# Kernel tuning notes

Measured on AMD Instinct MI355X. Metric: run time of the kernel, lower is better.

## Reference

```python
import jax, jax.numpy as jnp
import numpy as np

N_NODES = 100000
N_EDGES = 50000
NNZ = 1600000
D = 128
L = 2


def setup_inputs() -> dict:
    key = jax.random.key(0)
    ks = jax.random.split(key, 8)
    x = jax.random.normal(ks[0], (N_NODES, D), dtype=jnp.float32)
    e = jax.random.normal(ks[1], (N_EDGES, D), dtype=jnp.float32)
    node_idx = jax.random.randint(ks[2], (NNZ,), 0, N_NODES)
    edge_idx = jax.random.randint(ks[3], (NNZ,), 0, N_EDGES)
    hyperedge_index = jnp.stack([node_idx, edge_idx]).astype(jnp.int64)
    # per-layer params: node linear, edge linear, bias; shared PReLU slope a (init 0.25)
    Wn = jax.random.normal(ks[4], (L, D, D), dtype=jnp.float32) / np.sqrt(D)
    We = jax.random.normal(ks[5], (L, D, D), dtype=jnp.float32) / np.sqrt(D)
    b = jnp.zeros((L, D), dtype=jnp.float32)
    a = jnp.array(0.25, dtype=jnp.float32)
    return {"x": x, "e": e, "hyperedge_index": hyperedge_index,
            "num_nodes": N_NODES, "num_edges": N_EDGES,
            "Wn": Wn, "We": We, "b": b, "a": a}


def reference(x, e, hyperedge_index, num_nodes, num_edges, Wn, We, b, a):
    node_idx = hyperedge_index[0]
    edge_idx = hyperedge_index[1]
    ones = jnp.ones(node_idx.shape, x.dtype)
    deg_e = jax.ops.segment_sum(ones, edge_idx, num_segments=num_edges)  # B (edge degree)
    deg_v = jax.ops.segment_sum(ones, node_idx, num_segments=num_nodes)  # D_v (node degree)
    inv_e = jnp.where(deg_e > 0, 1.0 / deg_e, 0.0)[:, None]
    inv_v = jnp.where(deg_v > 0, 1.0 / deg_v, 0.0)[:, None]
    num_layers = Wn.shape[0]
    for l in range(num_layers):
        x1 = x @ Wn[l]                                   # [N, D]
        # gather node feats per incidence, mean-aggregate onto hyperedges
        m = jax.ops.segment_sum(x1[node_idx], edge_idx, num_segments=num_edges) * inv_e  # [E, D]
        h = m + e @ We[l] + b[l]                          # hyperedge hidden [E, D]
        # scatter hyperedge messages back to nodes, degree-normalized
        x = jax.ops.segment_sum(h[edge_idx], node_idx, num_segments=num_nodes) * inv_v   # [N, D]
        x = jnp.where(x >= 0, x, a * x)                   # shared PReLU
    return x
```

## Files before the change

### kernel.cpp

```cpp
#include <hip/hip_runtime.h>

#define DD 128


__global__ __launch_bounds__(256) void hist_kernel(const int* __restrict__ nidx,
                                                   const int* __restrict__ eidx,
                                                   int* __restrict__ cnt_v,
                                                   int* __restrict__ cnt_e, int nnz) {
  int i = blockIdx.x * 256 + threadIdx.x;
  if (i < nnz) {
    atomicAdd(&cnt_v[nidx[i]], 1);
    atomicAdd(&cnt_e[eidx[i]], 1);
  }
}

__global__ __launch_bounds__(256) void partial_reduce(const int* __restrict__ cnt, int n,
                                                      int* __restrict__ partials) {
  __shared__ int s[256];
  int t = threadIdx.x;
  int base = blockIdx.x * 1024;
  int sum = 0;
#pragma unroll
  for (int k = 0; k < 4; ++k) {
    int i = base + t * 4 + k;
    if (i < n) sum += cnt[i];
  }
  s[t] = sum;
  __syncthreads();
  for (int o = 128; o > 0; o >>= 1) {
    if (t < o) s[t] += s[t + o];
    __syncthreads();
  }
  if (t == 0) partials[blockIdx.x] = s[0];
}

__global__ __launch_bounds__(256) void scan_partials(int* __restrict__ partials, int nparts,
                                                     int* __restrict__ rp, int n) {
  __shared__ int s[256];
  int t = threadIdx.x;
  int v = (t < nparts) ? partials[t] : 0;
  s[t] = v;
  __syncthreads();
  for (int o = 1; o < 256; o <<= 1) {
    int add = (t >= o) ? s[t - o] : 0;
    __syncthreads();
    s[t] += add;
    __syncthreads();
  }
  if (t < nparts) partials[t] = s[t] - v;
  if (t == 255) rp[n] = s[255];
}

__global__ __launch_bounds__(256) void scan_final(const int* __restrict__ cnt,
                                                  const int* __restrict__ partials, int n,
                                                  int* __restrict__ rp, int* __restrict__ cur) {
  __shared__ int s[256];
  int t = threadIdx.x;
  int base = blockIdx.x * 1024;
  int v[4];
  int sum = 0;
#pragma unroll
  for (int k = 0; k < 4; ++k) {
    int i = base + t * 4 + k;
    v[k] = (i < n) ? cnt[i] : 0;
    sum += v[k];
  }
  s[t] = sum;
  __syncthreads();
  int own = sum;
  for (int o = 1; o < 256; o <<= 1) {
    int add = (t >= o) ? s[t - o] : 0;
    __syncthreads();
    s[t] += add;
    __syncthreads();
  }
  int off = partials[blockIdx.x] + (s[t] - own);
#pragma unroll
  for (int k = 0; k < 4; ++k) {
    int i = base + t * 4 + k;
    if (i < n) {
      rp[i] = off;
      cur[i] = off;
      off += v[k];
    }
  }
}

__global__ __launch_bounds__(256) void fill_kernel(const int* __restrict__ nidx,
                                                   const int* __restrict__ eidx,
                                                   int* __restrict__ cur_v,
                                                   int* __restrict__ cur_e,
                                                   int* __restrict__ col_v,
                                                   int* __restrict__ col_e, int nnz) {
  int i = blockIdx.x * 256 + threadIdx.x;
  if (i < nnz) {
    int v = nidx[i], e = eidx[i];
    int p = atomicAdd(&cur_e[e], 1);
    col_e[p] = v;
    int q = atomicAdd(&cur_v[v], 1);
    col_v[q] = e;
  }
}


__global__ __launch_bounds__(256) void gather_mean(const float* __restrict__ src,
                                                   const int* __restrict__ rp,
                                                   const int* __restrict__ col,
                                                   float* __restrict__ dst, int nrows) {
  int r = blockIdx.x * 4 + (threadIdx.x >> 6);
  if (r >= nrows) return;
  int lane = threadIdx.x & 63;
  int beg = rp[r], end = rp[r + 1];
  float ax = 0.f, ay = 0.f;
  int j = beg;
  for (; j + 4 <= end; j += 4) {
    int s0 = col[j], s1 = col[j + 1], s2 = col[j + 2], s3 = col[j + 3];
    float2 v0 = ((const float2*)(src + (size_t)s0 * DD))[lane];
    float2 v1 = ((const float2*)(src + (size_t)s1 * DD))[lane];
    float2 v2 = ((const float2*)(src + (size_t)s2 * DD))[lane];
    float2 v3 = ((const float2*)(src + (size_t)s3 * DD))[lane];
    ax += v0.x + v1.x + v2.x + v3.x;
    ay += v0.y + v1.y + v2.y + v3.y;
  }
  for (; j < end; ++j) {
    int s = col[j];
    float2 v = ((const float2*)(src + (size_t)s * DD))[lane];
    ax += v.x;
    ay += v.y;
  }
  float inv = (end > beg) ? 1.f / (float)(end - beg) : 0.f;
  float2 o;
  o.x = ax * inv;
  o.y = ay * inv;
  ((float2*)(dst + (size_t)r * DD))[lane] = o;
}

__global__ __launch_bounds__(256) void gather_prelu(const float* __restrict__ src,
                                                    const int* __restrict__ rp,
                                                    const int* __restrict__ col,
                                                    const float* __restrict__ a_ptr,
                                                    float* __restrict__ dst, int nrows) {
  int r = blockIdx.x * 4 + (threadIdx.x >> 6);
  if (r >= nrows) return;
  int lane = threadIdx.x & 63;
  int beg = rp[r], end = rp[r + 1];
  float ax = 0.f, ay = 0.f;
  int j = beg;
  for (; j + 4 <= end; j += 4) {
    int s0 = col[j], s1 = col[j + 1], s2 = col[j + 2], s3 = col[j + 3];
    float2 v0 = ((const float2*)(src + (size_t)s0 * DD))[lane];
    float2 v1 = ((const float2*)(src + (size_t)s1 * DD))[lane];
    float2 v2 = ((const float2*)(src + (size_t)s2 * DD))[lane];
    float2 v3 = ((const float2*)(src + (size_t)s3 * DD))[lane];
    ax += v0.x + v1.x + v2.x + v3.x;
    ay += v0.y + v1.y + v2.y + v3.y;
  }
  for (; j < end; ++j) {
    int s = col[j];
    float2 v = ((const float2*)(src + (size_t)s * DD))[lane];
    ax += v.x;
    ay += v.y;
  }
  float inv = (end > beg) ? 1.f / (float)(end - beg) : 0.f;
  float a = a_ptr[0];
  ax *= inv;
  ay *= inv;
  ax = ax >= 0.f ? ax : a * ax;
  ay = ay >= 0.f ? ay : a * ay;
  float2 o;
  o.x = ax;
  o.y = ay;
  ((float2*)(dst + (size_t)r * DD))[lane] = o;
}

__global__ __launch_bounds__(128) void edge_mlp(const float* __restrict__ agg,
                                                const float* __restrict__ ein,
                                                const float* __restrict__ Wn,
                                                const float* __restrict__ We,
                                                const float* __restrict__ bias,
                                                float* __restrict__ h, int E) {
  const int ROWS = 8;
  __shared__ float sA[ROWS][DD];
  __shared__ float sE[ROWS][DD];
  int r0 = blockIdx.x * ROWS;
  int t = threadIdx.x;
#pragma unroll
  for (int r = 0; r < ROWS; ++r) {
    int row = r0 + r;
    if (row < E) {
      sA[r][t] = agg[(size_t)row * DD + t];
      sE[r][t] = ein[(size_t)row * DD + t];
    } else {
      sA[r][t] = 0.f;
      sE[r][t] = 0.f;
    }
  }
  __syncthreads();

  float acc[ROWS];
  float bv = bias[t];
#pragma unroll
  for (int r = 0; r < ROWS; ++r) acc[r] = bv;

  for (int k = 0; k < DD; ++k) {
    float wn = Wn[k * DD + t];
    float we = We[k * DD + t];
#pragma unroll
    for (int r = 0; r < ROWS; ++r) {
      acc[r] += sA[r][k] * wn + sE[r][k] * we;
    }
  }
#pragma unroll
  for (int r = 0; r < ROWS; ++r) {
    int row = r0 + r;
    if (row < E) h[(size_t)row * DD + t] = acc[r];
  }
}


extern "C" void kernel_launch(void* const* d_in, const int* in_sizes, int n_in,
                              void* d_out, int out_size, void* d_ws, size_t ws_size,
                              hipStream_t stream) {
  const float* x_in  = (const float*)d_in[0];
  const float* e_in  = (const float*)d_in[1];
  const int*   hidx  = (const int*)d_in[2];
  const float* Wn    = (const float*)d_in[5];
  const float* We    = (const float*)d_in[6];
  const float* bias  = (const float*)d_in[7];
  const float* a_ptr = (const float*)d_in[8];

  const int N   = in_sizes[0] / DD;
  const int E   = in_sizes[1] / DD;
  const int NNZ = in_sizes[2] / 2;
  const int L   = in_sizes[5] / (DD * DD);

  const int* node_idx = hidx;
  const int* edge_idx = hidx + NNZ;

  char* ws = (char*)d_ws;
  size_t off = 0;
  auto take = [&](size_t bytes) {
    void* p = ws + off;
    off = (off + bytes + 511) & ~(size_t)511;
    return p;
  };
  int* cnt_v  = (int*)take((size_t)N * 4);
  int* cnt_e  = (int*)take((size_t)E * 4);
  int* rp_v   = (int*)take((size_t)(N + 1) * 4);
  int* rp_e   = (int*)take((size_t)(E + 1) * 4);
  int* cur_v  = (int*)take((size_t)N * 4);
  int* cur_e  = (int*)take((size_t)E * 4);
  int* part_v = (int*)take(256 * 4);
  int* part_e = (int*)take(256 * 4);
  int* col_v  = (int*)take((size_t)NNZ * 4);
  int* col_e  = (int*)take((size_t)NNZ * 4);
  float* agg  = (float*)take((size_t)E * DD * 4);

  float* xbuf = (float*)d_out;

  const int nparts_v = (N + 1023) / 1024;
  const int nparts_e = (E + 1023) / 1024;

  hipMemsetAsync(cnt_v, 0, (size_t)N * 4, stream);
  hipMemsetAsync(cnt_e, 0, (size_t)E * 4, stream);
  hist_kernel<<<(NNZ + 255) / 256, 256, 0, stream>>>(node_idx, edge_idx, cnt_v, cnt_e, NNZ);

  partial_reduce<<<nparts_v, 256, 0, stream>>>(cnt_v, N, part_v);
  partial_reduce<<<nparts_e, 256, 0, stream>>>(cnt_e, E, part_e);
  scan_partials<<<1, 256, 0, stream>>>(part_v, nparts_v, rp_v, N);
  scan_partials<<<1, 256, 0, stream>>>(part_e, nparts_e, rp_e, E);
  scan_final<<<nparts_v, 256, 0, stream>>>(cnt_v, part_v, N, rp_v, cur_v);
  scan_final<<<nparts_e, 256, 0, stream>>>(cnt_e, part_e, E, rp_e, cur_e);

  fill_kernel<<<(NNZ + 255) / 256, 256, 0, stream>>>(node_idx, edge_idx, cur_v, cur_e,
                                                     col_v, col_e, NNZ);

  const float* x_src = x_in;
  for (int l = 0; l < L; ++l) {
    gather_mean<<<(E + 3) / 4, 256, 0, stream>>>(x_src, rp_e, col_e, agg, E);
    edge_mlp<<<(E + 7) / 8, 128, 0, stream>>>(agg, e_in,
                                              Wn + (size_t)l * DD * DD,
                                              We + (size_t)l * DD * DD,
                                              bias + (size_t)l * DD, agg, E);
    gather_prelu<<<(N + 3) / 4, 256, 0, stream>>>(agg, rp_v, col_v, a_ptr, xbuf, N);
    x_src = xbuf;
  }
}
```

Before: 1.189 ms.

## Fuse edge gather-mean into edge MLP and vectorize CSR build kernels

Merges the per-edge mean aggregation with the edge linear layer into one kernel, so each block gathers 16 aggregated rows straight into shared memory and computes the 2x4 register-tiled matmul, dropping the agg round trip through global memory. The histogram and CSR fill kernels now read four indices per thread with int4 loads. Both gather loops unroll to eight independent loads in flight. The per-block work grows and fewer blocks launch for the edge stage, which may reduce latency hiding in the gather.

New measurement: 1.170 ms. Within noise of the previous version (-1.7%).

```diff
diff --git a/kernel.cpp b/kernel.cpp
--- a/kernel.cpp
+++ b/kernel.cpp
@@ -7,10 +7,23 @@
                                                    const int* __restrict__ eidx,
                                                    int* __restrict__ cnt_v,
                                                    int* __restrict__ cnt_e, int nnz) {
-  int i = blockIdx.x * 256 + threadIdx.x;
-  if (i < nnz) {
-    atomicAdd(&cnt_v[nidx[i]], 1);
-    atomicAdd(&cnt_e[eidx[i]], 1);
+  int base = (blockIdx.x * 256 + threadIdx.x) * 4;
+  if (base + 4 <= nnz) {
+    int4 n4 = *reinterpret_cast<const int4*>(nidx + base);
+    int4 e4 = *reinterpret_cast<const int4*>(eidx + base);
+    atomicAdd(&cnt_v[n4.x], 1);
+    atomicAdd(&cnt_v[n4.y], 1);
+    atomicAdd(&cnt_v[n4.z], 1);
+    atomicAdd(&cnt_v[n4.w], 1);
+    atomicAdd(&cnt_e[e4.x], 1);
+    atomicAdd(&cnt_e[e4.y], 1);
+    atomicAdd(&cnt_e[e4.z], 1);
+    atomicAdd(&cnt_e[e4.w], 1);
+  } else {
+    for (int i = base; i < nnz; ++i) {
+      atomicAdd(&cnt_v[nidx[i]], 1);
+      atomicAdd(&cnt_e[eidx[i]], 1);
+    }
   }
 }
 
@@ -92,47 +105,113 @@
                                                    int* __restrict__ cur_e,
                                                    int* __restrict__ col_v,
                                                    int* __restrict__ col_e, int nnz) {
-  int i = blockIdx.x * 256 + threadIdx.x;
-  if (i < nnz) {
-    int v = nidx[i], e = eidx[i];
-    int p = atomicAdd(&cur_e[e], 1);
-    col_e[p] = v;
-    int q = atomicAdd(&cur_v[v], 1);
-    col_v[q] = e;
-  }
-}
-
-
-__global__ __launch_bounds__(256) void gather_mean(const float* __restrict__ src,
-                                                   const int* __restrict__ rp,
-                                                   const int* __restrict__ col,
-                                                   float* __restrict__ dst, int nrows) {
-  int r = blockIdx.x * 4 + (threadIdx.x >> 6);
-  if (r >= nrows) return;
+  int base = (blockIdx.x * 256 + threadIdx.x) * 4;
+  if (base + 4 <= nnz) {
+    int4 n4 = *reinterpret_cast<const int4*>(nidx + base);
+    int4 e4 = *reinterpret_cast<const int4*>(eidx + base);
+    int p;
+    p = atomicAdd(&cur_e[e4.x], 1); col_e[p] = n4.x;
+    p = atomicAdd(&cur_e[e4.y], 1); col_e[p] = n4.y;
+    p = atomicAdd(&cur_e[e4.z], 1); col_e[p] = n4.z;
+    p = atomicAdd(&cur_e[e4.w], 1); col_e[p] = n4.w;
+    p = atomicAdd(&cur_v[n4.x], 1); col_v[p] = e4.x;
+    p = atomicAdd(&cur_v[n4.y], 1); col_v[p] = e4.y;
+    p = atomicAdd(&cur_v[n4.z], 1); col_v[p] = e4.z;
+    p = atomicAdd(&cur_v[n4.w], 1); col_v[p] = e4.w;
+  } else {
+    for (int i = base; i < nnz; ++i) {
+      int v = nidx[i], e = eidx[i];
+      int p = atomicAdd(&cur_e[e], 1);
+      col_e[p] = v;
+      int q = atomicAdd(&cur_v[v], 1);
+      col_v[q] = e;
+    }
+  }
+}
+
+__global__ __launch_bounds__(256) void gather_mlp(const float* __restrict__ x,
+                                                  const int* __restrict__ rp,
+                                                  const int* __restrict__ col,
+                                                  const float* __restrict__ ein,
+                                                  const float* __restrict__ Wn,
+                                                  const float* __restrict__ We,
+                                                  const float* __restrict__ bias,
+                                                  float* __restrict__ h, int E) {
+  const int ROWS = 16;
+  __shared__ float sA[ROWS][DD];
+  __shared__ float sE[ROWS][DD];
+  int r0 = blockIdx.x * ROWS;
+  int wave = threadIdx.x >> 6;
   int lane = threadIdx.x & 63;
-  int beg = rp[r], end = rp[r + 1];
-  float ax = 0.f, ay = 0.f;
-  int j = beg;
-  for (; j + 4 <= end; j += 4) {
-    int s0 = col[j], s1 = col[j + 1], s2 = col[j + 2], s3 = col[j + 3];
-    float2 v0 = ((const float2*)(src + (size_t)s0 * DD))[lane];
-    float2 v1 = ((const float2*)(src + (size_t)s1 * DD))[lane];
-    float2 v2 = ((const float2*)(src + (size_t)s2 * DD))[lane];
-    float2 v3 = ((const float2*)(src + (size_t)s3 * DD))[lane];
-    ax += v0.x + v1.x + v2.x + v3.x;
-    ay += v0.y + v1.y + v2.y + v3.y;
-  }
-  for (; j < end; ++j) {
-    int s = col[j];
-    float2 v = ((const float2*)(src + (size_t)s * DD))[lane];
-    ax += v.x;
-    ay += v.y;
-  }
-  float inv = (end > beg) ? 1.f / (float)(end - beg) : 0.f;
-  float2 o;
-  o.x = ax * inv;
-  o.y = ay * inv;
-  ((float2*)(dst + (size_t)r * DD))[lane] = o;
+
+#pragma unroll
+  for (int rr = 0; rr < 4; ++rr) {
+    int li = wave * 4 + rr;
+    int row = r0 + li;
+    float ax = 0.f, ay = 0.f;
+    float2 ev = make_float2(0.f, 0.f);
+    if (row < E) {
+      int beg = rp[row], end = rp[row + 1];
+      int j = beg;
+      for (; j + 8 <= end; j += 8) {
+        int c[8];
+#pragma unroll
+        for (int u = 0; u < 8; ++u) c[u] = col[j + u];
+#pragma unroll
+        for (int u = 0; u < 8; ++u) {
+          float2 v = ((const float2*)(x + (size_t)c[u] * DD))[lane];
+          ax += v.x;
+          ay += v.y;
+        }
+      }
+      for (; j < end; ++j) {
+        float2 v = ((const float2*)(x + (size_t)col[j] * DD))[lane];
+        ax += v.x;
+        ay += v.y;
+      }
+      float inv = (end > beg) ? 1.f / (float)(end - beg) : 0.f;
+      ax *= inv;
+      ay *= inv;
+      ev = ((const float2*)(ein + (size_t)row * DD))[lane];
+    }
+    ((float2*)&sA[li][0])[lane] = make_float2(ax, ay);
+    ((float2*)&sE[li][0])[lane] = ev;
+  }
+  __syncthreads();
+
+  int rg = threadIdx.x >> 5;
+  int rA = rg * 2, rB = rA + 1;
+  int c0 = (threadIdx.x & 31) * 4;
+  float acc0[4], acc1[4];
+#pragma unroll
+  for (int cc = 0; cc < 4; ++cc) {
+    float bv = bias[c0 + cc];
+    acc0[cc] = bv;
+    acc1[cc] = bv;
+  }
+  for (int k0 = 0; k0 < DD; k0 += 4) {
+    float aA[4], aB[4], eA[4], eB[4];
+    *(float4*)aA = *(const float4*)&sA[rA][k0];
+    *(float4*)aB = *(const float4*)&sA[rB][k0];
+    *(float4*)eA = *(const float4*)&sE[rA][k0];
+    *(float4*)eB = *(const float4*)&sE[rB][k0];
+#pragma unroll
+    for (int kk = 0; kk < 4; ++kk) {
+      float wn[4], we[4];
+      *(float4*)wn = *(const float4*)&Wn[(size_t)(k0 + kk) * DD + c0];
+      *(float4*)we = *(const float4*)&We[(size_t)(k0 + kk) * DD + c0];
+#pragma unroll
+      for (int cc = 0; cc < 4; ++cc) {
+        acc0[cc] += aA[kk] * wn[cc] + eA[kk] * we[cc];
+        acc1[cc] += aB[kk] * wn[cc] + eB[kk] * we[cc];
+      }
+    }
+  }
+  int rowA = r0 + rA, rowB = r0 + rB;
+  if (rowA < E)
+    *(float4*)&h[(size_t)rowA * DD + c0] = make_float4(acc0[0], acc0[1], acc0[2], acc0[3]);
+  if (rowB < E)
+    *(float4*)&h[(size_t)rowB * DD + c0] = make_float4(acc1[0], acc1[1], acc1[2], acc1[3]);
 }
 
 __global__ __launch_bounds__(256) void gather_prelu(const float* __restrict__ src,
@@ -146,18 +225,19 @@
   int beg = rp[r], end = rp[r + 1];
   float ax = 0.f, ay = 0.f;
   int j = beg;
-  for (; j + 4 <= end; j += 4) {
-    int s0 = col[j], s1 = col[j + 1], s2 = col[j + 2], s3 = col[j + 3];
-    float2 v0 = ((const float2*)(src + (size_t)s0 * DD))[lane];
-    float2 v1 = ((const float2*)(src + (size_t)s1 * DD))[lane];
-    float2 v2 = ((const float2*)(src + (size_t)s2 * DD))[lane];
-    float2 v3 = ((const float2*)(src + (size_t)s3 * DD))[lane];
-    ax += v0.x + v1.x + v2.x + v3.x;
-    ay += v0.y + v1.y + v2.y + v3.y;
+  for (; j + 8 <= end; j += 8) {
+    int c[8];
+#pragma unroll
+    for (int u = 0; u < 8; ++u) c[u] = col[j + u];
+#pragma unroll
+    for (int u = 0; u < 8; ++u) {
+      float2 v = ((const float2*)(src + (size_t)c[u] * DD))[lane];
+      ax += v.x;
+      ay += v.y;
+    }
   }
   for (; j < end; ++j) {
-    int s = col[j];
-    float2 v = ((const float2*)(src + (size_t)s * DD))[lane];
+    float2 v = ((const float2*)(src + (size_t)col[j] * DD))[lane];
     ax += v.x;
     ay += v.y;
   }
@@ -167,54 +247,7 @@
   ay *= inv;
   ax = ax >= 0.f ? ax : a * ax;
   ay = ay >= 0.f ? ay : a * ay;
-  float2 o;
-  o.x = ax;
-  o.y = ay;
-  ((float2*)(dst + (size_t)r * DD))[lane] = o;
-}
-
-__global__ __launch_bounds__(128) void edge_mlp(const float* __restrict__ agg,
-                                                const float* __restrict__ ein,
-                                                const float* __restrict__ Wn,
-                                                const float* __restrict__ We,
-                                                const float* __restrict__ bias,
-                                                float* __restrict__ h, int E) {
-  const int ROWS = 8;
-  __shared__ float sA[ROWS][DD];
-  __shared__ float sE[ROWS][DD];
-  int r0 = blockIdx.x * ROWS;
-  int t = threadIdx.x;
-#pragma unroll
-  for (int r = 0; r < ROWS; ++r) {
-    int row = r0 + r;
-    if (row < E) {
-      sA[r][t] = agg[(size_t)row * DD + t];
-      sE[r][t] = ein[(size_t)row * DD + t];
-    } else {
-      sA[r][t] = 0.f;
-      sE[r][t] = 0.f;
-    }
-  }
-  __syncthreads();
-
-  float acc[ROWS];
-  float bv = bias[t];
-#pragma unroll
-  for (int r = 0; r < ROWS; ++r) acc[r] = bv;
-
-  for (int k = 0; k < DD; ++k) {
-    float wn = Wn[k * DD + t];
-    float we = We[k * DD + t];
-#pragma unroll
-    for (int r = 0; r < ROWS; ++r) {
-      acc[r] += sA[r][k] * wn + sE[r][k] * we;
-    }
-  }
-#pragma unroll
-  for (int r = 0; r < ROWS; ++r) {
-    int row = r0 + r;
-    if (row < E) h[(size_t)row * DD + t] = acc[r];
-  }
+  ((float2*)(dst + (size_t)r * DD))[lane] = make_float2(ax, ay);
 }
 
 
@@ -254,16 +287,17 @@
   int* part_e = (int*)take(256 * 4);
   int* col_v  = (int*)take((size_t)NNZ * 4);
   int* col_e  = (int*)take((size_t)NNZ * 4);
-  float* agg  = (float*)take((size_t)E * DD * 4);
+  float* hbuf = (float*)take((size_t)E * DD * 4);
 
   float* xbuf = (float*)d_out;
 
   const int nparts_v = (N + 1023) / 1024;
   const int nparts_e = (E + 1023) / 1024;
+  const int nnz4 = (NNZ + 3) / 4;
 
   hipMemsetAsync(cnt_v, 0, (size_t)N * 4, stream);
   hipMemsetAsync(cnt_e, 0, (size_t)E * 4, stream);
-  hist_kernel<<<(NNZ + 255) / 256, 256, 0, stream>>>(node_idx, edge_idx, cnt_v, cnt_e, NNZ);
+  hist_kernel<<<(nnz4 + 255) / 256, 256, 0, stream>>>(node_idx, edge_idx, cnt_v, cnt_e, NNZ);
 
   partial_reduce<<<nparts_v, 256, 0, stream>>>(cnt_v, N, part_v);
   partial_reduce<<<nparts_e, 256, 0, stream>>>(cnt_e, E, part_e);
@@ -272,17 +306,16 @@
   scan_final<<<nparts_v, 256, 0, stream>>>(cnt_v, part_v, N, rp_v, cur_v);
   scan_final<<<nparts_e, 256, 0, stream>>>(cnt_e, part_e, E, rp_e, cur_e);
 
-  fill_kernel<<<(NNZ + 255) / 256, 256, 0, stream>>>(node_idx, edge_idx, cur_v, cur_e,
-                                                     col_v, col_e, NNZ);
+  fill_kernel<<<(nnz4 + 255) / 256, 256, 0, stream>>>(node_idx, edge_idx, cur_v, cur_e,
+                                                      col_v, col_e, NNZ);
 
   const float* x_src = x_in;
   for (int l = 0; l < L; ++l) {
-    gather_mean<<<(E + 3) / 4, 256, 0, stream>>>(x_src, rp_e, col_e, agg, E);
-    edge_mlp<<<(E + 7) / 8, 128, 0, stream>>>(agg, e_in,
-                                              Wn + (size_t)l * DD * DD,
-                                              We + (size_t)l * DD * DD,
-                                              bias + (size_t)l * DD, agg, E);
-    gather_prelu<<<(N + 3) / 4, 256, 0, stream>>>(agg, rp_v, col_v, a_ptr, xbuf, N);
+    gather_mlp<<<(E + 15) / 16, 256, 0, stream>>>(x_src, rp_e, col_e, e_in,
+                                                  Wn + (size_t)l * DD * DD,
+                                                  We + (size_t)l * DD * DD,
+                                                  bias + (size_t)l * DD, hbuf, E);
+    gather_prelu<<<(N + 3) / 4, 256, 0, stream>>>(hbuf, rp_v, col_v, a_ptr, xbuf, N);
     x_src = xbuf;
   }
 }
```
